# Kernel optimization log

Hardware: AMD Instinct MI355X
Metric: run time of the kernel (lower is better)

## Reference

```python
import jax, jax.numpy as jnp
import numpy as np


def _boxsum(x):
    # x: [C, H, W] -> depthwise 3x3 all-ones sum conv, SAME padding (ChannelWiseSum(C, 3))
    C = x.shape[0]
    k = jnp.ones((C, 1, 3, 3), x.dtype)
    y = jax.lax.conv_general_dilated(
        x[None], k, window_strides=(1, 1), padding='SAME',
        dimension_numbers=('NCHW', 'OIHW', 'NCHW'), feature_group_count=C)
    return y[0]


def setup_inputs() -> dict:
    key = jax.random.key(0)
    k1, k2 = jax.random.split(key)
    H = W = 4096
    rgb = jax.random.uniform(k1, (3, H, W), dtype=jnp.float32)
    # alpha in [0,1] with ~half the pixels exactly 0 so the border diffusion is exercised
    a = jax.random.uniform(k2, (1, H, W), dtype=jnp.float32) * 2.0 - 1.0
    alpha = jnp.maximum(a, 0.0)
    return {"rgb": rgb, "alpha": alpha, "offset": 16}


def reference(rgb, alpha, offset):
    # rgb: [3,H,W], alpha: [1,H,W], offset: python int (number of diffusion steps)
    mask = (alpha > 0.0).astype(rgb.dtype)           # [1,H,W]
    rgb = rgb * mask

    def step(carry, _):
        rgb, mask = carry
        mask_nega = jnp.abs(mask - 1.0)              # [1,H,W], broadcasts over channels
        mask_weight = _boxsum(mask)                  # [1,H,W]
        border = _boxsum(rgb) / (mask_weight + 1e-7) # [3,H,W]
        border = border * mask_nega
        rgb = rgb * mask + border
        mask = (mask_weight > 0.0).astype(rgb.dtype)
        return (rgb, mask), None

    (rgb, _), _ = jax.lax.scan(step, (rgb, mask), None, length=offset)
    return jnp.clip(rgb, 0.0, 1.0)
```

## Files before the change

### kernel.cpp

```cpp
#include <hip/hip_runtime.h>

constexpr int W = 4096;
constexpr int H = 4096;
constexpr int HW = W * H;

constexpr int BX = 64, BY = 4;
constexpr int TILE_W = BX * 4;
constexpr int GRID_X = W / TILE_W;
constexpr int GRID_Y = H / BY;

typedef unsigned char u8;
typedef unsigned int u32;

__device__ __forceinline__ float clamp01(float v) { return fminf(fmaxf(v, 0.f), 1.f); }
__device__ __forceinline__ float4 ld4(const float* p) { return *reinterpret_cast<const float4*>(p); }
__device__ __forceinline__ void st4(float* p, float4 v) { *reinterpret_cast<float4*>(p) = v; }
__device__ __forceinline__ float4 z4() { return make_float4(0.f, 0.f, 0.f, 0.f); }
__device__ __forceinline__ float rcp_f(float x) { return __builtin_amdgcn_rcpf(x); }

__device__ __attribute__((noinline)) u32 far_distance(
    const float* __restrict__ alpha, int x, int y)
{
    for (int dy = -2; dy <= 2; ++dy) {
        int yy = y + dy;
        if (yy < 0 || yy >= H) continue;
        if (dy == -2 || dy == 2) {
            for (int dx = -2; dx <= 2; ++dx) {
                int xx = x + dx;
                if (xx < 0 || xx >= W) continue;
                if (alpha[yy * W + xx] > 0.f) return 2;
            }
        } else {
            if (x - 2 >= 0 && alpha[yy * W + x - 2] > 0.f) return 2;
            if (x + 2 < W && alpha[yy * W + x + 2] > 0.f) return 2;
        }
    }
    for (int r = 3; r <= 16; ++r) {
        bool f = false;
        for (int dx = -r; dx <= r && !f; ++dx) {
            int gx = x + dx;
            if (gx < 0 || gx >= W) continue;
            int gy = y - r;
            if (gy >= 0 && alpha[gy * W + gx] > 0.f) f = true;
            gy = y + r;
            if (!f && gy < H && alpha[gy * W + gx] > 0.f) f = true;
        }
        for (int dy = -r + 1; dy <= r - 1 && !f; ++dy) {
            int gy = y + dy;
            if (gy < 0 || gy >= H) continue;
            int gx = x - r;
            if (gx >= 0 && alpha[gy * W + gx] > 0.f) f = true;
            gx = x + r;
            if (!f && gx < W && alpha[gy * W + gx] > 0.f) f = true;
        }
        if (f) return r;
    }
    return 255;
}

__device__ __forceinline__ float4 vsum4(float4 u, float4 c, float4 d,
                                        float4 mU, float4 mC, float4 mD)
{
    float4 r;
    r.x = u.x * mU.x + c.x * mC.x + d.x * mD.x;
    r.y = u.y * mU.y + c.y * mC.y + d.y * mD.y;
    r.z = u.z * mU.z + c.z * mC.z + d.z * mD.z;
    r.w = u.w * mU.w + c.w * mC.w + d.w * mD.w;
    return r;
}

__global__ __launch_bounds__(BX * BY) void pass1_kernel(
    const float* __restrict__ rgb, const float* __restrict__ alpha,
    float* __restrict__ out, u8* __restrict__ dmap,
    u32* __restrict__ cnt, int* __restrict__ list, u32 cap)
{
    const int tx = threadIdx.x;
    const int ty = threadIdx.y;
    const int x0 = blockIdx.x * TILE_W + tx * 4;
    const int y  = blockIdx.y * BY + ty;
    const int p0 = y * W + x0;
    const bool up = (y > 0), dn = (y < H - 1);

    const float* Gp = rgb + HW;
    const float* Bp = rgb + 2 * HW;

    float4 aU = up ? ld4(alpha + p0 - W) : z4();
    float4 aC = ld4(alpha + p0);
    float4 aD = dn ? ld4(alpha + p0 + W) : z4();
    float4 rU = up ? ld4(rgb + p0 - W) : z4();
    float4 rC = ld4(rgb + p0);
    float4 rD = dn ? ld4(rgb + p0 + W) : z4();
    float4 gU = up ? ld4(Gp + p0 - W) : z4();
    float4 gC = ld4(Gp + p0);
    float4 gD = dn ? ld4(Gp + p0 + W) : z4();
    float4 bU = up ? ld4(Bp + p0 - W) : z4();
    float4 bC = ld4(Bp + p0);
    float4 bD = dn ? ld4(Bp + p0 + W) : z4();

    float4 mU = make_float4(aU.x > 0.f, aU.y > 0.f, aU.z > 0.f, aU.w > 0.f);
    float4 mC = make_float4(aC.x > 0.f, aC.y > 0.f, aC.z > 0.f, aC.w > 0.f);
    float4 mD = make_float4(aD.x > 0.f, aD.y > 0.f, aD.z > 0.f, aD.w > 0.f);

    float4 vw;
    vw.x = mU.x + mC.x + mD.x;
    vw.y = mU.y + mC.y + mD.y;
    vw.z = mU.z + mC.z + mD.z;
    vw.w = mU.w + mC.w + mD.w;
    float4 vr = vsum4(rU, rC, rD, mU, mC, mD);
    float4 vg = vsum4(gU, gC, gD, mU, mC, mD);
    float4 vb = vsum4(bU, bC, bD, mU, mC, mD);

    float lw = __shfl_up(vw.w, 1), rw = __shfl_down(vw.x, 1);
    float lr = __shfl_up(vr.w, 1), rr = __shfl_down(vr.x, 1);
    float lg = __shfl_up(vg.w, 1), rg = __shfl_down(vg.x, 1);
    float lb = __shfl_up(vb.w, 1), rb = __shfl_down(vb.x, 1);

    if (tx == 0 || tx == BX - 1) {
        int xh = (tx == 0) ? x0 - 1 : x0 + 4;
        float hr = 0.f, hg = 0.f, hb = 0.f, hw = 0.f;
        if (xh >= 0 && xh < W) {
            #pragma unroll
            for (int dy = -1; dy <= 1; ++dy) {
                int yy = y + dy;
                if (yy < 0 || yy >= H) continue;
                int q = yy * W + xh;
                float m = (alpha[q] > 0.f) ? 1.f : 0.f;
                hw += m;
                hr += m * rgb[q];
                hg += m * Gp[q];
                hb += m * Bp[q];
            }
        }
        if (tx == 0) { lw = hw; lr = hr; lg = hg; lb = hb; }
        else         { rw = hw; rr = hr; rg = hg; rb = hb; }
    }

    float sw[4] = { lw + vw.x + vw.y, vw.x + vw.y + vw.z,
                    vw.y + vw.z + vw.w, vw.z + vw.w + rw };
    float sr[4] = { lr + vr.x + vr.y, vr.x + vr.y + vr.z,
                    vr.y + vr.z + vr.w, vr.z + vr.w + rr };
    float sg[4] = { lg + vg.x + vg.y, vg.x + vg.y + vg.z,
                    vg.y + vg.z + vg.w, vg.z + vg.w + rg };
    float sb[4] = { lb + vb.x + vb.y, vb.x + vb.y + vb.z,
                    vb.y + vb.z + vb.w, vb.z + vb.w + rb };

    const float mca[4] = {mC.x, mC.y, mC.z, mC.w};
    const float rca[4] = {rC.x, rC.y, rC.z, rC.w};
    const float gca[4] = {gC.x, gC.y, gC.z, gC.w};
    const float bca[4] = {bC.x, bC.y, bC.z, bC.w};

    float o_r[4], o_g[4], o_b[4];
    u32 dv[4];

    #pragma unroll
    for (int i = 0; i < 4; ++i) {
        if (mca[i] > 0.f) {
            dv[i] = 0;
            o_r[i] = rca[i]; o_g[i] = gca[i]; o_b[i] = bca[i];
        } else if (sw[i] > 0.f) {
            dv[i] = 1;
            float inv = rcp_f(sw[i] + 1e-7f);
            o_r[i] = sr[i] * inv; o_g[i] = sg[i] * inv; o_b[i] = sb[i] * inv;
        } else {
            u32 d = far_distance(alpha, x0 + i, y);
            dv[i] = d;
            o_r[i] = 0.f; o_g[i] = 0.f; o_b[i] = 0.f;
            if (d >= 3 && d <= 16) {
                u32 idx = atomicAdd(cnt, 1u);
                if (idx < cap) list[idx] = p0 + i;
            }
        }
    }

    st4(out + p0, make_float4(clamp01(o_r[0]), clamp01(o_r[1]),
                              clamp01(o_r[2]), clamp01(o_r[3])));
    st4(out + HW + p0, make_float4(clamp01(o_g[0]), clamp01(o_g[1]),
                                   clamp01(o_g[2]), clamp01(o_g[3])));
    st4(out + 2 * HW + p0, make_float4(clamp01(o_b[0]), clamp01(o_b[1]),
                                       clamp01(o_b[2]), clamp01(o_b[3])));
    *reinterpret_cast<uchar4*>(dmap + p0) =
        make_uchar4((u8)dv[0], (u8)dv[1], (u8)dv[2], (u8)dv[3]);
}

__device__ __forceinline__ void fill_pixel(float* __restrict__ out,
                                           const u8* __restrict__ dmap,
                                           int x, int y, int t)
{
    float s0 = 0.f, s1 = 0.f, s2 = 0.f;
    int cnt = 0;
    #pragma unroll
    for (int dy = -1; dy <= 1; ++dy) {
        int ny = y + dy;
        if (ny < 0 || ny >= H) continue;
        #pragma unroll
        for (int dx = -1; dx <= 1; ++dx) {
            int nx = x + dx;
            if (nx < 0 || nx >= W) continue;
            int q = ny * W + nx;
            if (dmap[q] == (u8)(t - 1)) {
                cnt++;
                s0 += out[q];
                s1 += out[HW + q];
                s2 += out[2 * HW + q];
            }
        }
    }
    float inv = rcp_f((float)cnt + 1e-7f);
    int p = y * W + x;
    out[p]          = clamp01(s0 * inv);
    out[HW + p]     = clamp01(s1 * inv);
    out[2 * HW + p] = clamp01(s2 * inv);
}

__device__ __forceinline__ u32 has_byte2(u32 x) {
    u32 v = x ^ 0x02020202u;
    return (v - 0x01010101u) & ~v & 0x80808080u;
}

__global__ __launch_bounds__(256) void tail_dense(
    float* __restrict__ out, const u8* __restrict__ dmap)
{
    int idx = blockIdx.x * 256 + threadIdx.x;
    int p = idx * 16;
    uint4 dq = *reinterpret_cast<const uint4*>(dmap + p);
    if (!(has_byte2(dq.x) | has_byte2(dq.y) | has_byte2(dq.z) | has_byte2(dq.w)))
        return;
    int y = p >> 12;
    int xb = p & (W - 1);
    u32 words[4] = {dq.x, dq.y, dq.z, dq.w};
    #pragma unroll
    for (int wi = 0; wi < 4; ++wi) {
        u32 v = words[wi];
        #pragma unroll
        for (int b = 0; b < 4; ++b) {
            if (((v >> (8 * b)) & 0xFFu) == 2u)
                fill_pixel(out, dmap, xb + wi * 4 + b, y, 2);
        }
    }
}

__global__ __launch_bounds__(256) void tail_far(
    float* __restrict__ out, const u8* __restrict__ dmap,
    const int* __restrict__ list, const u32* __restrict__ cnt, u32 cap)
{
    u32 n = *cnt;
    if (n > cap) n = cap;
    for (int t = 3; t <= 16; ++t) {
        for (u32 i = threadIdx.x; i < n; i += 256) {
            int p = list[i];
            if (dmap[p] == (u8)t)
                fill_pixel(out, dmap, p & (W - 1), p >> 12, t);
        }
        __syncthreads();
    }
}

extern "C" void kernel_launch(void* const* d_in, const int* in_sizes, int n_in,
                              void* d_out, int out_size, void* d_ws, size_t ws_size,
                              hipStream_t stream) {
    const float* rgb   = (const float*)d_in[0];
    const float* alpha = (const float*)d_in[1];
    float* out = (float*)d_out;

    u8* dmap  = (u8*)d_ws;
    u32* cnt  = (u32*)((char*)d_ws + HW);
    int* list = (int*)((char*)d_ws + HW + 16);
    u32 cap = 0;
    if (ws_size > (size_t)HW + 16) {
        size_t c = (ws_size - HW - 16) / 4;
        cap = (u32)(c > (1u << 22) ? (1u << 22) : c);
    }

    hipMemsetAsync(cnt, 0, 4, stream);

    pass1_kernel<<<dim3(GRID_X, GRID_Y), dim3(BX, BY), 0, stream>>>(
        rgb, alpha, out, dmap, cnt, list, cap);
    tail_dense<<<HW / 16 / 256, 256, 0, stream>>>(out, dmap);
    tail_far<<<1, 256, 0, stream>>>(out, dmap, list, cnt, cap);
}
```

Baseline: 158.3 us.

## Drop distance map, sweep multiple rows per thread, and list-drive tail passes

Removes the per-pixel u8 distance map write and the full-image dense tail scan. The tail passes are now driven by compact lists of distance-2 and farther pixels, and distance is recomputed from alpha when needed. Each thread now handles 4 rows using a 6-row register window, which cuts redundant vertical halo loads from 3x to 1.5x. In exchange it uses more registers and recomputes alpha neighbourhoods in the tails, and it adds another atomic counter.

```diff
diff --git a/kernel.cpp b/kernel.cpp
--- a/kernel.cpp
+++ b/kernel.cpp
@@ -5,9 +5,11 @@
 constexpr int HW = W * H;
 
 constexpr int BX = 64, BY = 4;
+constexpr int ROWS = 4;
 constexpr int TILE_W = BX * 4;
+constexpr int TILE_H = BY * ROWS;
 constexpr int GRID_X = W / TILE_W;
-constexpr int GRID_Y = H / BY;
+constexpr int GRID_Y = H / TILE_H;
 
 typedef unsigned char u8;
 typedef unsigned int u32;
@@ -15,8 +17,19 @@
 __device__ __forceinline__ float clamp01(float v) { return fminf(fmaxf(v, 0.f), 1.f); }
 __device__ __forceinline__ float4 ld4(const float* p) { return *reinterpret_cast<const float4*>(p); }
 __device__ __forceinline__ void st4(float* p, float4 v) { *reinterpret_cast<float4*>(p) = v; }
-__device__ __forceinline__ float4 z4() { return make_float4(0.f, 0.f, 0.f, 0.f); }
 __device__ __forceinline__ float rcp_f(float x) { return __builtin_amdgcn_rcpf(x); }
+
+__device__ __forceinline__ float4 f4add3(float4 a, float4 b, float4 c) {
+    return make_float4(a.x + b.x + c.x, a.y + b.y + c.y,
+                       a.z + b.z + c.z, a.w + b.w + c.w);
+}
+__device__ __forceinline__ float4 f4msum3(float4 a, float4 ma, float4 b, float4 mb,
+                                          float4 c, float4 mc) {
+    return make_float4(a.x * ma.x + b.x * mb.x + c.x * mc.x,
+                       a.y * ma.y + b.y * mb.y + c.y * mc.y,
+                       a.z * ma.z + b.z * mb.z + c.z * mc.z,
+                       a.w * ma.w + b.w * mb.w + c.w * mc.w);
+}
 
 __device__ __attribute__((noinline)) u32 far_distance(
     const float* __restrict__ alpha, int x, int y)
@@ -58,198 +71,229 @@
     return 255;
 }
 
-__device__ __forceinline__ float4 vsum4(float4 u, float4 c, float4 d,
-                                        float4 mU, float4 mC, float4 mD)
-{
-    float4 r;
-    r.x = u.x * mU.x + c.x * mC.x + d.x * mD.x;
-    r.y = u.y * mU.y + c.y * mC.y + d.y * mD.y;
-    r.z = u.z * mU.z + c.z * mC.z + d.z * mD.z;
-    r.w = u.w * mU.w + c.w * mC.w + d.w * mD.w;
-    return r;
+__device__ u32 d_of(const float* __restrict__ alpha, int x, int y) {
+    if (alpha[y * W + x] > 0.f) return 0;
+    for (int dy = -1; dy <= 1; ++dy) {
+        int yy = y + dy;
+        if (yy < 0 || yy >= H) continue;
+        for (int dx = -1; dx <= 1; ++dx) {
+            int xx = x + dx;
+            if (xx < 0 || xx >= W) continue;
+            if (alpha[yy * W + xx] > 0.f) return 1;
+        }
+    }
+    return far_distance(alpha, x, y);
 }
 
 __global__ __launch_bounds__(BX * BY) void pass1_kernel(
     const float* __restrict__ rgb, const float* __restrict__ alpha,
-    float* __restrict__ out, u8* __restrict__ dmap,
-    u32* __restrict__ cnt, int* __restrict__ list, u32 cap)
+    float* __restrict__ out,
+    u32* __restrict__ cnts, u32* __restrict__ list2, u32 cap2,
+    u32* __restrict__ list3, u32 cap3)
 {
     const int tx = threadIdx.x;
     const int ty = threadIdx.y;
     const int x0 = blockIdx.x * TILE_W + tx * 4;
-    const int y  = blockIdx.y * BY + ty;
-    const int p0 = y * W + x0;
-    const bool up = (y > 0), dn = (y < H - 1);
+    const int ytop = blockIdx.y * TILE_H + ty * ROWS;
 
     const float* Gp = rgb + HW;
     const float* Bp = rgb + 2 * HW;
 
-    float4 aU = up ? ld4(alpha + p0 - W) : z4();
-    float4 aC = ld4(alpha + p0);
-    float4 aD = dn ? ld4(alpha + p0 + W) : z4();
-    float4 rU = up ? ld4(rgb + p0 - W) : z4();
-    float4 rC = ld4(rgb + p0);
-    float4 rD = dn ? ld4(rgb + p0 + W) : z4();
-    float4 gU = up ? ld4(Gp + p0 - W) : z4();
-    float4 gC = ld4(Gp + p0);
-    float4 gD = dn ? ld4(Gp + p0 + W) : z4();
-    float4 bU = up ? ld4(Bp + p0 - W) : z4();
-    float4 bC = ld4(Bp + p0);
-    float4 bD = dn ? ld4(Bp + p0 + W) : z4();
-
-    float4 mU = make_float4(aU.x > 0.f, aU.y > 0.f, aU.z > 0.f, aU.w > 0.f);
-    float4 mC = make_float4(aC.x > 0.f, aC.y > 0.f, aC.z > 0.f, aC.w > 0.f);
-    float4 mD = make_float4(aD.x > 0.f, aD.y > 0.f, aD.z > 0.f, aD.w > 0.f);
-
-    float4 vw;
-    vw.x = mU.x + mC.x + mD.x;
-    vw.y = mU.y + mC.y + mD.y;
-    vw.z = mU.z + mC.z + mD.z;
-    vw.w = mU.w + mC.w + mD.w;
-    float4 vr = vsum4(rU, rC, rD, mU, mC, mD);
-    float4 vg = vsum4(gU, gC, gD, mU, mC, mD);
-    float4 vb = vsum4(bU, bC, bD, mU, mC, mD);
-
-    float lw = __shfl_up(vw.w, 1), rw = __shfl_down(vw.x, 1);
-    float lr = __shfl_up(vr.w, 1), rr = __shfl_down(vr.x, 1);
-    float lg = __shfl_up(vg.w, 1), rg = __shfl_down(vg.x, 1);
-    float lb = __shfl_up(vb.w, 1), rb = __shfl_down(vb.x, 1);
-
+    int off[6];
+    float yval[6];
+    #pragma unroll
+    for (int j = 0; j < 6; ++j) {
+        int yy = ytop - 1 + j;
+        int yc = yy < 0 ? 0 : (yy >= H ? H - 1 : yy);
+        off[j] = yc * W + x0;
+        yval[j] = (yy >= 0 && yy < H) ? 1.f : 0.f;
+    }
+
+    float4 a[6], r_[6], g_[6], b_[6];
+    #pragma unroll
+    for (int j = 0; j < 6; ++j) a[j] = ld4(alpha + off[j]);
+    #pragma unroll
+    for (int j = 0; j < 6; ++j) r_[j] = ld4(rgb + off[j]);
+    #pragma unroll
+    for (int j = 0; j < 6; ++j) g_[j] = ld4(Gp + off[j]);
+    #pragma unroll
+    for (int j = 0; j < 6; ++j) b_[j] = ld4(Bp + off[j]);
+
+    float4 m[6];
+    #pragma unroll
+    for (int j = 0; j < 6; ++j)
+        m[j] = make_float4((a[j].x > 0.f) ? yval[j] : 0.f,
+                           (a[j].y > 0.f) ? yval[j] : 0.f,
+                           (a[j].z > 0.f) ? yval[j] : 0.f,
+                           (a[j].w > 0.f) ? yval[j] : 0.f);
+
+    float hw[ROWS], hr[ROWS], hg[ROWS], hb[ROWS];
+    #pragma unroll
+    for (int r = 0; r < ROWS; ++r) { hw[r] = hr[r] = hg[r] = hb[r] = 0.f; }
     if (tx == 0 || tx == BX - 1) {
         int xh = (tx == 0) ? x0 - 1 : x0 + 4;
-        float hr = 0.f, hg = 0.f, hb = 0.f, hw = 0.f;
         if (xh >= 0 && xh < W) {
+            int dxh = xh - x0;
+            float am[6], rv[6], gv[6], bv[6];
             #pragma unroll
+            for (int j = 0; j < 6; ++j) {
+                am[j] = (alpha[off[j] + dxh] > 0.f) ? yval[j] : 0.f;
+                rv[j] = rgb[off[j] + dxh];
+                gv[j] = Gp[off[j] + dxh];
+                bv[j] = Bp[off[j] + dxh];
+            }
+            #pragma unroll
+            for (int r = 0; r < ROWS; ++r) {
+                hw[r] = am[r] + am[r + 1] + am[r + 2];
+                hr[r] = rv[r] * am[r] + rv[r + 1] * am[r + 1] + rv[r + 2] * am[r + 2];
+                hg[r] = gv[r] * am[r] + gv[r + 1] * am[r + 1] + gv[r + 2] * am[r + 2];
+                hb[r] = bv[r] * am[r] + bv[r + 1] * am[r + 1] + bv[r + 2] * am[r + 2];
+            }
+        }
+    }
+
+    #pragma unroll
+    for (int r = 0; r < ROWS; ++r) {
+        float4 vw = f4add3(m[r], m[r + 1], m[r + 2]);
+        float4 vr = f4msum3(r_[r], m[r], r_[r + 1], m[r + 1], r_[r + 2], m[r + 2]);
+        float4 vg = f4msum3(g_[r], m[r], g_[r + 1], m[r + 1], g_[r + 2], m[r + 2]);
+        float4 vb = f4msum3(b_[r], m[r], b_[r + 1], m[r + 1], b_[r + 2], m[r + 2]);
+
+        float lw = __shfl_up(vw.w, 1), rw = __shfl_down(vw.x, 1);
+        float lr = __shfl_up(vr.w, 1), rr = __shfl_down(vr.x, 1);
+        float lg = __shfl_up(vg.w, 1), rg = __shfl_down(vg.x, 1);
+        float lb = __shfl_up(vb.w, 1), rb = __shfl_down(vb.x, 1);
+        if (tx == 0)      { lw = hw[r]; lr = hr[r]; lg = hg[r]; lb = hb[r]; }
+        if (tx == BX - 1) { rw = hw[r]; rr = hr[r]; rg = hg[r]; rb = hb[r]; }
+
+        float swv[4] = { lw + vw.x + vw.y, vw.x + vw.y + vw.z,
+                         vw.y + vw.z + vw.w, vw.z + vw.w + rw };
+        float srv[4] = { lr + vr.x + vr.y, vr.x + vr.y + vr.z,
+                         vr.y + vr.z + vr.w, vr.z + vr.w + rr };
+        float sgv[4] = { lg + vg.x + vg.y, vg.x + vg.y + vg.z,
+                         vg.y + vg.z + vg.w, vg.z + vg.w + rg };
+        float sbv[4] = { lb + vb.x + vb.y, vb.x + vb.y + vb.z,
+                         vb.y + vb.z + vb.w, vb.z + vb.w + rb };
+
+        const float mc[4]  = { m[r + 1].x, m[r + 1].y, m[r + 1].z, m[r + 1].w };
+        const float cr[4]  = { r_[r + 1].x, r_[r + 1].y, r_[r + 1].z, r_[r + 1].w };
+        const float cg[4]  = { g_[r + 1].x, g_[r + 1].y, g_[r + 1].z, g_[r + 1].w };
+        const float cb[4]  = { b_[r + 1].x, b_[r + 1].y, b_[r + 1].z, b_[r + 1].w };
+
+        const int prow = (ytop + r) * W + x0;
+        float o0[4], o1[4], o2[4];
+
+        #pragma unroll
+        for (int i = 0; i < 4; ++i) {
+            if (mc[i] > 0.f) {
+                o0[i] = cr[i]; o1[i] = cg[i]; o2[i] = cb[i];
+            } else if (swv[i] > 0.f) {
+                float inv = rcp_f(swv[i] + 1e-7f);
+                o0[i] = srv[i] * inv; o1[i] = sgv[i] * inv; o2[i] = sbv[i] * inv;
+            } else {
+                o0[i] = 0.f; o1[i] = 0.f; o2[i] = 0.f;
+                u32 d = far_distance(alpha, x0 + i, ytop + r);
+                if (d == 2) {
+                    u32 idx = atomicAdd(&cnts[0], 1u);
+                    if (idx < cap2) list2[idx] = (u32)(prow + i);
+                } else if (d <= 16) {
+                    u32 idx = atomicAdd(&cnts[1], 1u);
+                    if (idx < cap3) list3[idx] = (u32)(prow + i) | (d << 24);
+                }
+            }
+        }
+
+        st4(out + prow, make_float4(clamp01(o0[0]), clamp01(o0[1]),
+                                    clamp01(o0[2]), clamp01(o0[3])));
+        st4(out + HW + prow, make_float4(clamp01(o1[0]), clamp01(o1[1]),
+                                         clamp01(o1[2]), clamp01(o1[3])));
+        st4(out + 2 * HW + prow, make_float4(clamp01(o2[0]), clamp01(o2[1]),
+                                             clamp01(o2[2]), clamp01(o2[3])));
+    }
+}
+
+__global__ __launch_bounds__(256) void tail2_kernel(
+    const float* __restrict__ alpha, float* __restrict__ out,
+    const u32* __restrict__ cnts, const u32* __restrict__ list2, u32 cap2)
+{
+    u32 n = cnts[0];
+    if (n > cap2) n = cap2;
+    for (u32 idx = blockIdx.x * 256u + threadIdx.x; idx < n;
+         idx += gridDim.x * 256u) {
+        u32 p = list2[idx];
+        int y = (int)(p >> 12), x = (int)(p & (W - 1));
+
+        float mw[5][5];
+        #pragma unroll
+        for (int dy = -2; dy <= 2; ++dy) {
+            int yy = y + dy;
+            bool vy = (yy >= 0) && (yy < H);
+            #pragma unroll
+            for (int dx = -2; dx <= 2; ++dx) {
+                int xx = x + dx;
+                bool v = vy && (xx >= 0) && (xx < W);
+                mw[dy + 2][dx + 2] = v ? ((alpha[yy * W + xx] > 0.f) ? 1.f : 0.f) : 0.f;
+            }
+        }
+
+        float s0 = 0.f, s1 = 0.f, s2 = 0.f, cw = 0.f;
+        #pragma unroll
+        for (int dy = -1; dy <= 1; ++dy) {
+            #pragma unroll
+            for (int dx = -1; dx <= 1; ++dx) {
+                int qx = x + dx, qy = y + dy;
+                if (qx < 0 || qx >= W || qy < 0 || qy >= H) continue;
+                float any =
+                    mw[dy + 1][dx + 1] + mw[dy + 1][dx + 2] + mw[dy + 1][dx + 3] +
+                    mw[dy + 2][dx + 1] + mw[dy + 2][dx + 2] + mw[dy + 2][dx + 3] +
+                    mw[dy + 3][dx + 1] + mw[dy + 3][dx + 2] + mw[dy + 3][dx + 3];
+                if (any > 0.f) {
+                    int q = qy * W + qx;
+                    cw += 1.f;
+                    s0 += out[q]; s1 += out[HW + q]; s2 += out[2 * HW + q];
+                }
+            }
+        }
+        float inv = rcp_f(cw + 1e-7f);
+        int pp = y * W + x;
+        out[pp]          = clamp01(s0 * inv);
+        out[HW + pp]     = clamp01(s1 * inv);
+        out[2 * HW + pp] = clamp01(s2 * inv);
+    }
+}
+
+__global__ __launch_bounds__(256) void tail3_kernel(
+    const float* __restrict__ alpha, float* __restrict__ out,
+    const u32* __restrict__ cnts, const u32* __restrict__ list3, u32 cap3)
+{
+    u32 n = cnts[1];
+    if (n > cap3) n = cap3;
+    if (n == 0) return;
+    for (int t = 3; t <= 16; ++t) {
+        for (u32 i = threadIdx.x; i < n; i += 256u) {
+            u32 e = list3[i];
+            if ((e >> 24) != (u32)t) continue;
+            int p = (int)(e & 0xFFFFFFu);
+            int y = p >> 12, x = p & (W - 1);
+            float s0 = 0.f, s1 = 0.f, s2 = 0.f, cw = 0.f;
             for (int dy = -1; dy <= 1; ++dy) {
-                int yy = y + dy;
-                if (yy < 0 || yy >= H) continue;
-                int q = yy * W + xh;
-                float m = (alpha[q] > 0.f) ? 1.f : 0.f;
-                hw += m;
-                hr += m * rgb[q];
-                hg += m * Gp[q];
-                hb += m * Bp[q];
-            }
-        }
-        if (tx == 0) { lw = hw; lr = hr; lg = hg; lb = hb; }
-        else         { rw = hw; rr = hr; rg = hg; rb = hb; }
-    }
-
-    float sw[4] = { lw + vw.x + vw.y, vw.x + vw.y + vw.z,
-                    vw.y + vw.z + vw.w, vw.z + vw.w + rw };
-    float sr[4] = { lr + vr.x + vr.y, vr.x + vr.y + vr.z,
-                    vr.y + vr.z + vr.w, vr.z + vr.w + rr };
-    float sg[4] = { lg + vg.x + vg.y, vg.x + vg.y + vg.z,
-                    vg.y + vg.z + vg.w, vg.z + vg.w + rg };
-    float sb[4] = { lb + vb.x + vb.y, vb.x + vb.y + vb.z,
-                    vb.y + vb.z + vb.w, vb.z + vb.w + rb };
-
-    const float mca[4] = {mC.x, mC.y, mC.z, mC.w};
-    const float rca[4] = {rC.x, rC.y, rC.z, rC.w};
-    const float gca[4] = {gC.x, gC.y, gC.z, gC.w};
-    const float bca[4] = {bC.x, bC.y, bC.z, bC.w};
-
-    float o_r[4], o_g[4], o_b[4];
-    u32 dv[4];
-
-    #pragma unroll
-    for (int i = 0; i < 4; ++i) {
-        if (mca[i] > 0.f) {
-            dv[i] = 0;
-            o_r[i] = rca[i]; o_g[i] = gca[i]; o_b[i] = bca[i];
-        } else if (sw[i] > 0.f) {
-            dv[i] = 1;
-            float inv = rcp_f(sw[i] + 1e-7f);
-            o_r[i] = sr[i] * inv; o_g[i] = sg[i] * inv; o_b[i] = sb[i] * inv;
-        } else {
-            u32 d = far_distance(alpha, x0 + i, y);
-            dv[i] = d;
-            o_r[i] = 0.f; o_g[i] = 0.f; o_b[i] = 0.f;
-            if (d >= 3 && d <= 16) {
-                u32 idx = atomicAdd(cnt, 1u);
-                if (idx < cap) list[idx] = p0 + i;
-            }
-        }
-    }
-
-    st4(out + p0, make_float4(clamp01(o_r[0]), clamp01(o_r[1]),
-                              clamp01(o_r[2]), clamp01(o_r[3])));
-    st4(out + HW + p0, make_float4(clamp01(o_g[0]), clamp01(o_g[1]),
-                                   clamp01(o_g[2]), clamp01(o_g[3])));
-    st4(out + 2 * HW + p0, make_float4(clamp01(o_b[0]), clamp01(o_b[1]),
-                                       clamp01(o_b[2]), clamp01(o_b[3])));
-    *reinterpret_cast<uchar4*>(dmap + p0) =
-        make_uchar4((u8)dv[0], (u8)dv[1], (u8)dv[2], (u8)dv[3]);
-}
-
-__device__ __forceinline__ void fill_pixel(float* __restrict__ out,
-                                           const u8* __restrict__ dmap,
-                                           int x, int y, int t)
-{
-    float s0 = 0.f, s1 = 0.f, s2 = 0.f;
-    int cnt = 0;
-    #pragma unroll
-    for (int dy = -1; dy <= 1; ++dy) {
-        int ny = y + dy;
-        if (ny < 0 || ny >= H) continue;
-        #pragma unroll
-        for (int dx = -1; dx <= 1; ++dx) {
-            int nx = x + dx;
-            if (nx < 0 || nx >= W) continue;
-            int q = ny * W + nx;
-            if (dmap[q] == (u8)(t - 1)) {
-                cnt++;
-                s0 += out[q];
-                s1 += out[HW + q];
-                s2 += out[2 * HW + q];
-            }
-        }
-    }
-    float inv = rcp_f((float)cnt + 1e-7f);
-    int p = y * W + x;
-    out[p]          = clamp01(s0 * inv);
-    out[HW + p]     = clamp01(s1 * inv);
-    out[2 * HW + p] = clamp01(s2 * inv);
-}
-
-__device__ __forceinline__ u32 has_byte2(u32 x) {
-    u32 v = x ^ 0x02020202u;
-    return (v - 0x01010101u) & ~v & 0x80808080u;
-}
-
-__global__ __launch_bounds__(256) void tail_dense(
-    float* __restrict__ out, const u8* __restrict__ dmap)
-{
-    int idx = blockIdx.x * 256 + threadIdx.x;
-    int p = idx * 16;
-    uint4 dq = *reinterpret_cast<const uint4*>(dmap + p);
-    if (!(has_byte2(dq.x) | has_byte2(dq.y) | has_byte2(dq.z) | has_byte2(dq.w)))
-        return;
-    int y = p >> 12;
-    int xb = p & (W - 1);
-    u32 words[4] = {dq.x, dq.y, dq.z, dq.w};
-    #pragma unroll
-    for (int wi = 0; wi < 4; ++wi) {
-        u32 v = words[wi];
-        #pragma unroll
-        for (int b = 0; b < 4; ++b) {
-            if (((v >> (8 * b)) & 0xFFu) == 2u)
-                fill_pixel(out, dmap, xb + wi * 4 + b, y, 2);
-        }
-    }
-}
-
-__global__ __launch_bounds__(256) void tail_far(
-    float* __restrict__ out, const u8* __restrict__ dmap,
-    const int* __restrict__ list, const u32* __restrict__ cnt, u32 cap)
-{
-    u32 n = *cnt;
-    if (n > cap) n = cap;
-    for (int t = 3; t <= 16; ++t) {
-        for (u32 i = threadIdx.x; i < n; i += 256) {
-            int p = list[i];
-            if (dmap[p] == (u8)t)
-                fill_pixel(out, dmap, p & (W - 1), p >> 12, t);
+                int qy = y + dy;
+                if (qy < 0 || qy >= H) continue;
+                for (int dx = -1; dx <= 1; ++dx) {
+                    int qx = x + dx;
+                    if (qx < 0 || qx >= W) continue;
+                    if (dx == 0 && dy == 0) continue;
+                    if (d_of(alpha, qx, qy) == (u32)(t - 1)) {
+                        int q = qy * W + qx;
+                        cw += 1.f;
+                        s0 += out[q]; s1 += out[HW + q]; s2 += out[2 * HW + q];
+                    }
+                }
+            }
+            float inv = rcp_f(cw + 1e-7f);
+            out[p]          = clamp01(s0 * inv);
+            out[HW + p]     = clamp01(s1 * inv);
+            out[2 * HW + p] = clamp01(s2 * inv);
         }
         __syncthreads();
     }
@@ -262,19 +306,21 @@
     const float* alpha = (const float*)d_in[1];
     float* out = (float*)d_out;
 
-    u8* dmap  = (u8*)d_ws;
-    u32* cnt  = (u32*)((char*)d_ws + HW);
-    int* list = (int*)((char*)d_ws + HW + 16);
-    u32 cap = 0;
-    if (ws_size > (size_t)HW + 16) {
-        size_t c = (ws_size - HW - 16) / 4;
-        cap = (u32)(c > (1u << 22) ? (1u << 22) : c);
-    }
-
-    hipMemsetAsync(cnt, 0, 4, stream);
+    u32* cnts  = (u32*)d_ws;
+    u32* list2 = (u32*)((char*)d_ws + 64);
+    u32 cap2 = 1u << 20, cap3 = 1u << 16;
+    size_t need = 64 + (size_t)cap2 * 4 + (size_t)cap3 * 4;
+    if (ws_size < need) {
+        size_t avail = ws_size > 64 ? (ws_size - 64) / 4 : 0;
+        cap3 = (u32)(avail / 8);
+        cap2 = (u32)(avail - cap3);
+    }
+    u32* list3 = list2 + cap2;
+
+    hipMemsetAsync(cnts, 0, 8, stream);
 
     pass1_kernel<<<dim3(GRID_X, GRID_Y), dim3(BX, BY), 0, stream>>>(
-        rgb, alpha, out, dmap, cnt, list, cap);
-    tail_dense<<<HW / 16 / 256, 256, 0, stream>>>(out, dmap);
-    tail_far<<<1, 256, 0, stream>>>(out, dmap, list, cnt, cap);
-}
+        rgb, alpha, out, cnts, list2, cap2, list3, cap3);
+    tail2_kernel<<<256, 256, 0, stream>>>(alpha, out, cnts, list2, cap2);
+    tail3_kernel<<<1, 256, 0, stream>>>(alpha, out, cnts, list3, cap3);
+}
```

Measured after the change: 409.7 us. 159% more time.
